# Kernel tuning notes

Measured on AMD Instinct MI355X. Metric: run time of the kernel, lower is better.

## Reference

```python
import jax, jax.numpy as jnp
import numpy as np

B, CLS, C, H, HP, WP, K = 16, 20, 512, 4, 32, 32, 9
G = H * CLS  # grapher channels = 80
EPS = 1e-5
BNS = 1.0 / np.sqrt(1.0 + EPS)  # eval-mode BN, running_mean=0, running_var=1


def _bn(x, g, b, axis):
    shape = [1] * x.ndim
    shape[axis] = -1
    return x * (g * BNS).reshape(shape) + b.reshape(shape)


def setup_inputs():
    key = jax.random.key(0)
    ks = jax.random.split(key, 16)
    def rn(k, shp, scale=0.02):
        return jax.random.normal(k, shp, dtype=jnp.float32) * scale
    return {
        "x_cls": jax.random.normal(ks[0], (B, CLS, C), jnp.float32),
        "x_patch": jax.random.normal(ks[1], (B, C, HP, WP), jnp.float32),
        "norm_x_w": jnp.ones((C, 1, 1), jnp.float32),
        "norm_x_b": jnp.zeros((C, 1, 1), jnp.float32),
        "pq_w": rn(ks[2], (C, C)), "pq_b": rn(ks[3], (C,)),
        "ncls_w": jnp.ones((C,), jnp.float32), "ncls_b": jnp.zeros((C,), jnp.float32),
        "pkv_w": rn(ks[4], (2 * C, C)), "pkv_b": rn(ks[5], (2 * C,)),
        "fc1_w": rn(ks[6], (G, G)), "fc1_b": rn(ks[7], (G,)),
        "bn1_g": jnp.ones((G,), jnp.float32), "bn1_b": jnp.zeros((G,), jnp.float32),
        "mr_w": rn(ks[8], (2 * G, 2 * G // H)), "mr_b": rn(ks[9], (2 * G,)),
        "bn2_g": jnp.ones((2 * G,), jnp.float32), "bn2_b": jnp.zeros((2 * G,), jnp.float32),
        "fc2_w": rn(ks[10], (G, 2 * G)), "fc2_b": rn(ks[11], (G,)),
        "bn3_g": jnp.ones((G,), jnp.float32), "bn3_b": jnp.zeros((G,), jnp.float32),
        "proj_w": rn(ks[12], (C, C)), "proj_b": rn(ks[13], (C,)),
    }


def _forward(x_cls, x_patch, norm_x_w, norm_x_b, pq_w, pq_b, ncls_w, ncls_b,
             pkv_w, pkv_b, fc1_w, fc1_b, bn1_g, bn1_b, mr_w, mr_b, bn2_g, bn2_b,
             fc2_w, fc2_b, bn3_g, bn3_b, proj_w, proj_b):
    hd = C // H
    N = HP * WP
    scale = hd ** -0.5
    # norm_x: LayerNormGeneral over (C,H,W)
    c0 = x_patch - x_patch.mean(axis=(1, 2, 3), keepdims=True)
    s0 = (c0 * c0).mean(axis=(1, 2, 3), keepdims=True)
    xn = c0 / jnp.sqrt(s0 + EPS) * norm_x_w + norm_x_b
    # proj_q (1x1 conv) -> multi-head query [B,H,N,hd]
    q = jnp.einsum('oc,bchw->bohw', pq_w, xn) + pq_b[None, :, None, None]
    q = q.reshape(B, H, hd, N).transpose(0, 1, 3, 2)
    # norm_cls: LayerNorm over channel dim
    m = x_cls.mean(-1, keepdims=True)
    v = ((x_cls - m) ** 2).mean(-1, keepdims=True)
    xc = (x_cls - m) / jnp.sqrt(v + EPS) * ncls_w + ncls_b
    kv = xc @ pkv_w.T + pkv_b                                  # [B,Cls,2C]
    k_, v_ = kv[..., :C], kv[..., C:]
    key_ = k_.reshape(B, CLS, H, hd).transpose(0, 2, 3, 1)     # [B,H,hd,Cls]
    val = v_.reshape(B, CLS, H, hd).transpose(0, 2, 1, 3)      # [B,H,Cls,hd]
    attn = jnp.einsum('bhnd,bhdc->bhnc', q, key_) * scale      # [B,H,N,Cls]
    amap = attn.reshape(B, H, HP, WP, CLS).transpose(0, 1, 4, 2, 3).reshape(B, G, HP, WP)
    # ---- Grapher (ViG gcn_lib): fc1 -> DyGraphConv(MRConv, KNN) -> fc2 -> residual ----
    sc = amap
    x = jnp.einsum('oc,bchw->bohw', fc1_w, amap) + fc1_b[None, :, None, None]
    x = _bn(x, bn1_g, bn1_b, 1)
    xf = x.reshape(B, G, N).transpose(0, 2, 1)                 # [B,N,G]
    # dense KNN on L2-normalized features (indices only, non-diff)
    xu = xf / jnp.maximum(jnp.linalg.norm(xf, axis=-1, keepdims=True), 1e-12)
    sq = jnp.sum(xu * xu, axis=-1)                             # [B,N]
    neg_d = 2.0 * jnp.einsum('bnc,bmc->bnm', xu, xu) - sq[:, :, None] - sq[:, None, :]
    _, nn_idx = jax.lax.top_k(neg_d, K)                        # [B,N,K]
    neigh = xf[jnp.arange(B)[:, None, None], nn_idx]           # [B,N,K,G]
    xj = jnp.max(neigh - xf[:, :, None, :], axis=2)            # [B,N,G] max-relative
    y = jnp.stack([xf, xj], axis=-1).reshape(B, N, 2 * G)      # interleave (x0,xj0,x1,...)
    # grouped 1x1 conv (groups=H), BN, GELU
    yg = y.reshape(B, N, H, 2 * G // H)
    wg = mr_w.reshape(H, 2 * G // H, 2 * G // H)
    z = jnp.einsum('bngi,goi->bngo', yg, wg).reshape(B, N, 2 * G) + mr_b
    z = _bn(z, bn2_g, bn2_b, 2)
    z = jax.nn.gelu(z, approximate=False)
    z2 = z @ fc2_w.T + fc2_b                                   # [B,N,G]
    z2 = _bn(z2, bn3_g, bn3_b, 2)
    gout = z2.transpose(0, 2, 1).reshape(B, G, HP, WP) + sc
    # ---- softmax-weighted value aggregation ----
    attn2 = gout.reshape(B, H, CLS, N).transpose(0, 1, 3, 2)   # [B,H,N,Cls]
    attn2 = jax.nn.softmax(attn2, axis=-1)
    out = jnp.einsum('bhnc,bhcd->bhnd', attn2, val)            # [B,H,N,hd]
    out = out.transpose(0, 1, 3, 2).reshape(B, C, HP, WP)
    out = jnp.einsum('oc,bchw->bohw', proj_w, out) + proj_b[None, :, None, None]
    return x_patch + out


def reference(x_cls, x_patch, norm_x_w, norm_x_b, pq_w, pq_b, ncls_w, ncls_b,
              pkv_w, pkv_b, fc1_w, fc1_b, bn1_g, bn1_b, mr_w, mr_b, bn2_g, bn2_b,
              fc2_w, fc2_b, bn3_g, bn3_b, proj_w, proj_b):
    return _forward(x_cls, x_patch, norm_x_w, norm_x_b, pq_w, pq_b, ncls_w, ncls_b,
                    pkv_w, pkv_b, fc1_w, fc1_b, bn1_g, bn1_b, mr_w, mr_b, bn2_g, bn2_b,
                    fc2_w, fc2_b, bn3_g, bn3_b, proj_w, proj_b)
```

## Files before the change

### kernel.cpp

```cpp
#include <hip/hip_runtime.h>
#include <math.h>

#define DI __device__ __forceinline__

constexpr int B_ = 16, CLS_ = 20, C_ = 512, H_ = 4, HD_ = 128, N_ = 1024, G_ = 80, G2_ = 160, K_ = 9;
constexpr float EPS_ = 1e-5f;
constexpr float BNS_ = 0.9999950000374997f;
constexpr float SCALE_ = 0.08838834764831845f;
constexpr float INVSQRT2_ = 0.7071067811865475f;

typedef __attribute__((ext_vector_type(8))) short bf16x8;
typedef __attribute__((ext_vector_type(4))) float f32x4;

constexpr long OFF_PART  = 0;
constexpr long OFF_EB    = 4096;
constexpr long OFF_EBB   = OFF_EB    + 524288;
constexpr long OFF_KV    = OFF_EBB   + 2048;
constexpr long OFF_AMAPT = OFF_KV    + 327680;
constexpr long OFF_XF    = OFF_AMAPT + 1310720;
constexpr long OFF_XUB   = OFF_XF    + 1310720;
constexpr long OFF_W1BD  = OFF_XUB   + 786432;
constexpr long OFF_FC2B  = OFF_W1BD  + 16384;
constexpr long OFF_SQ    = OFF_FC2B  + 8192;
constexpr long OFF_NEGD  = OFF_SQ    + 16384;
constexpr long OFF_GOUTT = OFF_NEGD  + 16777216 + 147456;
constexpr long OFF_WPB   = OFF_GOUTT + 1310720;
constexpr long OFF_Y     = OFF_WPB   + 131072;
constexpr long OFF_FC1B  = OFF_Y     + 1310720;
constexpr long OFF_PB    = OFF_FC1B  + 4096;

DI float wsum(float v){
#pragma unroll
  for(int d=1; d<64; d<<=1) v += __shfl_xor(v, d);
  return v;
}
DI unsigned short f2b(float f){
  unsigned u = __float_as_uint(f);
  unsigned r = (u + 0x7FFFu + ((u >> 16) & 1u)) >> 16;
  return (unsigned short)r;
}

#define GLOAD16(g, s) __builtin_amdgcn_global_load_lds((const __attribute__((address_space(1))) void*)(g), \
                        (__attribute__((address_space(3))) void*)(s), 16, 0, 0)

__global__ __launch_bounds__(256) void k_pre(const float* __restrict__ x, float* __restrict__ part,
                                             const float* __restrict__ xcls,
                                             const float* __restrict__ ncw, const float* __restrict__ ncb,
                                             const float* __restrict__ pkvw, const float* __restrict__ pkvb,
                                             float* __restrict__ kv,
                                             const float* __restrict__ projw, unsigned short* __restrict__ wpb,
                                             const float* __restrict__ mrw, const float* __restrict__ fc2w,
                                             const float* __restrict__ fc1w,
                                             unsigned short* __restrict__ w1bd, unsigned short* __restrict__ fc2b16,
                                             unsigned short* __restrict__ fc1b16){
  __shared__ float sh[CLS_*C_];
  int blk = blockIdx.x, t = threadIdx.x;
  if(blk < 1024){
    const float4* xp = (const float4*)x;
    long base4 = (long)blk * 2048;
    float s = 0.f, ss = 0.f;
#pragma unroll
    for(int j=0;j<8;++j){
      float4 v = xp[base4 + t + 256*j];
      s  += v.x + v.y + v.z + v.w;
      ss += v.x*v.x + v.y*v.y + v.z*v.z + v.w*v.w;
    }
    s = wsum(s); ss = wsum(ss);
    int wv = t >> 6;
    if((t & 63) == 0){ sh[wv] = s; sh[4+wv] = ss; }
    __syncthreads();
    if(t == 0){
      part[blk*2]   = sh[0]+sh[1]+sh[2]+sh[3];
      part[blk*2+1] = sh[4]+sh[5]+sh[6]+sh[7];
    }
    return;
  }
  if(blk < 1152){
    int idx = blk - 1024;
    int b = idx >> 3, ochunk = idx & 7;
    float (*xc)[C_] = (float(*)[C_])sh;
    int wv = t >> 6, l = t & 63;
    for(int cls = wv; cls < CLS_; cls += 4){
      const float* xr = xcls + ((long)b*CLS_ + cls) * C_;
      float vals[8];
      float s = 0.f, ss = 0.f;
#pragma unroll
      for(int j=0;j<8;++j){ float v = xr[l + 64*j]; vals[j] = v; s += v; ss += v*v; }
      s = wsum(s); ss = wsum(ss);
      float m = s / (float)C_;
      float var = ss / (float)C_ - m*m;
      float inv = 1.0f / sqrtf(var + EPS_);
#pragma unroll
      for(int j=0;j<8;++j){
        int c = l + 64*j;
        xc[cls][c] = (vals[j]-m)*inv*ncw[c] + ncb[c];
      }
    }
    __syncthreads();
    int o = ochunk*128 + (t & 127);
    int cls0 = (t >> 7) * 10;
    float acc[10] = {};
    const float* wrow = pkvw + (long)o * C_;
    for(int k4 = 0; k4 < C_; k4 += 4){
      float4 w4 = *(const float4*)&wrow[k4];
#pragma unroll
      for(int i=0;i<10;++i){
        acc[i] += w4.x*xc[cls0+i][k4] + w4.y*xc[cls0+i][k4+1] + w4.z*xc[cls0+i][k4+2] + w4.w*xc[cls0+i][k4+3];
      }
    }
    float bo = pkvb[o];
#pragma unroll
    for(int i=0;i<10;++i) kv[((long)b*CLS_ + cls0+i)*1024 + o] = acc[i] + bo;
    return;
  }
  int blk2 = blk - 1152;
  if(blk2 < 256){
    long i = (long)blk2*256 + t;
    float4 v = ((const float4*)projw)[i];
    uint2 o;
    o.x = (unsigned)f2b(v.x) | ((unsigned)f2b(v.y) << 16);
    o.y = (unsigned)f2b(v.z) | ((unsigned)f2b(v.w) << 16);
    ((uint2*)wpb)[i] = o;
    return;
  }
  int row = blk2 - 256;
  if(row < 160){
    if(t < 160){
      unsigned short v = 0;
      if(t/40 == row/40) v = f2b(mrw[row*40 + (t % 40)]);
      w1bd[row*160 + t] = v;
    }
  } else if(row < 240){
    if(t < 160) fc2b16[(row-160)*160 + t] = f2b(fc2w[(long)(row-160)*160 + t]);
  } else if(row < 320){
    int r = row - 240;
    if(t < 96) fc1b16[r*96 + t] = (t < G_) ? f2b(fc1w[(long)r*G_ + t]) : (unsigned short)0;
  }
}

__global__ __launch_bounds__(256) void k_eprep(const float* __restrict__ kv, const float* __restrict__ pqw,
                                               const float* __restrict__ pqb, const float* __restrict__ partbuf,
                                               const float* __restrict__ nw, const float* __restrict__ nbv,
                                               unsigned short* __restrict__ Eb, float* __restrict__ ebb,
                                               float* __restrict__ pb){
  int b = blockIdx.x, hh = blockIdx.y, cch = blockIdx.z, t = threadIdx.x;
  if(hh == 4){
    if(cch == 0){
      unsigned* z = (unsigned*)(Eb + ((long)b*128 + 80)*512);
      for(int i=t; i<12288; i+=256) z[i] = 0;
    }
    return;
  }
  __shared__ float sst[2];
  __shared__ float key[CLS_][HD_];
  __shared__ float part[4][CLS_][64];
  if(t < 64){
    float s  = partbuf[(b*64+t)*2];
    float ss = partbuf[(b*64+t)*2+1];
    s = wsum(s); ss = wsum(ss);
    if(t == 0){
      const float cnt = (float)(C_ * N_);
      float m = s / cnt;
      sst[0] = m;
      sst[1] = 1.0f / sqrtf(ss / cnt - m*m + EPS_);
    }
  }
  int h = hh, c0 = cch*64;
  for(int i=t; i<CLS_*HD_; i+=256){
    int cls = i >> 7, d = i & 127;
    key[cls][d] = kv[((long)b*CLS_+cls)*1024 + h*HD_ + d];
  }
  __syncthreads();
  float m = sst[0], inv = sst[1];
  int c = t & 63, ds = t >> 6;
  float acc[CLS_] = {};
  const float* wp = pqw + ((long)(h*HD_ + ds*32))*C_ + c0 + c;
#pragma unroll 8
  for(int di=0; di<32; ++di){
    float wv = wp[(long)di*C_];
#pragma unroll
    for(int cls=0; cls<CLS_; ++cls) acc[cls] += key[cls][ds*32+di]*wv;
  }
#pragma unroll
  for(int cls=0; cls<CLS_; ++cls) part[ds][cls][c] = acc[cls];
  __syncthreads();
  for(int i=t; i<CLS_*64; i+=256){
    int cls = i >> 6, cc = i & 63;
    float v = (part[0][cls][cc]+part[1][cls][cc]+part[2][cls][cc]+part[3][cls][cc]) * SCALE_;
    int cg = c0 + cc;
    float a = inv * nw[cg];
    float bbv = nbv[cg] - m*a;
    Eb[((long)b*128 + h*CLS_ + cls)*512 + cg] = f2b(v*a);
    part[0][cls][cc] = v*bbv;
  }
  __syncthreads();
  if(t < CLS_){
    float s = 0.f;
    for(int cc=0; cc<64; ++cc) s += part[0][t][cc];
    pb[((long)b*8 + cch)*G_ + t < 0 ? 0 : ((long)b*8 + cch)*G_ + h*CLS_ + t] = s;
  }
  if(cch == 0 && t >= 64 && t < 64 + CLS_){
    int tt = t - 64;
    float bacc = 0.f;
    for(int d=0; d<HD_; ++d) bacc += key[tt][d]*pqb[h*HD_+d];
    ebb[b*G_ + h*CLS_ + tt] = bacc*SCALE_;
  }
}

__global__ __launch_bounds__(256) void k_amap_fc1(const unsigned short* __restrict__ Eb,
                                                  const float* __restrict__ xp,
                                                  const float* __restrict__ ebb,
                                                  const float* __restrict__ pb,
                                                  const unsigned short* __restrict__ w1b,
                                                  const float* __restrict__ f1bias,
                                                  const float* __restrict__ g1, const float* __restrict__ b1,
                                                  float* __restrict__ amapT,
                                                  float* __restrict__ xf, unsigned short* __restrict__ xub,
                                                  float* __restrict__ sq){
  __shared__ unsigned short Xl[64*520];
  __shared__ unsigned short Bgl[4096];
  unsigned short* A1 = Xl;
  int b = blockIdx.y, n0 = blockIdx.x*64;
  int t = threadIdx.x, w = t >> 6, l = t & 63;
  int wr = w >> 1, wc = w & 1;
  {
    int nb = t & 7, cl = t >> 3;
    const float* xb = xp + (long)b*C_*N_ + n0 + nb*8;
#pragma unroll 4
    for(int pass=0; pass<16; ++pass){
      int c = pass*32 + cl;
      const float* src = xb + (long)c*N_;
      float4 v0 = *(const float4*)src;
      float4 v1 = *(const float4*)(src+4);
      int base = (nb*8)*520 + c;
      Xl[base         ] = f2b(v0.x);
      Xl[base + 520   ] = f2b(v0.y);
      Xl[base + 520*2 ] = f2b(v0.z);
      Xl[base + 520*3 ] = f2b(v0.w);
      Xl[base + 520*4 ] = f2b(v1.x);
      Xl[base + 520*5 ] = f2b(v1.y);
      Xl[base + 520*6 ] = f2b(v1.z);
      Xl[base + 520*7 ] = f2b(v1.w);
    }
  }
  __syncthreads();
  f32x4 acc[2][4] = {};
  const unsigned short* Bt = Eb + ((long)b*128 + w*16 + (l>>2))*512 + (l&3)*8;
  int ra = wr*32 + (l & 15);
  int rb = wc*64 + (l & 15);
  int kq = (l >> 4) * 8;
  for(int k0 = 0; k0 < 512; k0 += 32){
    if(k0) __syncthreads();
    GLOAD16(Bt + k0,          &Bgl[w*512]);
    GLOAD16(Bt + 64*512 + k0, &Bgl[2048 + w*512]);
    __syncthreads();
    bf16x8 af[2], bfr[4];
#pragma unroll
    for(int rt=0; rt<2; ++rt) af[rt]  = *(const bf16x8*)&Xl[(ra + rt*16)*520 + k0 + kq];
#pragma unroll
    for(int ct=0; ct<4; ++ct) bfr[ct] = *(const bf16x8*)&Bgl[(rb + ct*16)*32 + kq];
#pragma unroll
    for(int rt=0; rt<2; ++rt)
#pragma unroll
      for(int ct=0; ct<4; ++ct)
        acc[rt][ct] = __builtin_amdgcn_mfma_f32_16x16x32_bf16(af[rt], bfr[ct], acc[rt][ct], 0, 0, 0);
  }
  float bias4[4];
#pragma unroll
  for(int ct=0; ct<4; ++ct){
    int g = wc*64 + ct*16 + (l & 15);
    float bi = 0.f;
    if(g < G_){
      bi = ebb[b*G_ + g];
#pragma unroll
      for(int cc=0; cc<8; ++cc) bi += pb[((long)b*8 + cc)*G_ + g];
    }
    bias4[ct] = bi;
  }
  __syncthreads();
  int r0 = (l >> 4)*4;
#pragma unroll
  for(int rt=0; rt<2; ++rt){
#pragma unroll
    for(int r=0; r<4; ++r){
      int lrow = wr*32 + rt*16 + r0 + r;
      long rowb = ((long)b*N_ + n0 + lrow)*G_;
#pragma unroll
      for(int ct=0; ct<4; ++ct){
        int g = wc*64 + ct*16 + (l & 15);
        if(g < G_){
          float val = acc[rt][ct][r] + bias4[ct];
          amapT[rowb + g] = val;
          A1[lrow*96 + g] = f2b(val);
        } else if(g < 96){
          A1[lrow*96 + g] = 0;
        }
      }
    }
  }
  __syncthreads();
  int lr = l & 15, lk = l >> 4;
  bf16x8 ay[3];
  const unsigned short* arow = &A1[(w*16 + lr)*96 + lk*8];
#pragma unroll
  for(int ks=0; ks<3; ++ks) ay[ks] = *(const bf16x8*)&arow[ks*32];
  f32x4 acc5[5] = {};
  const unsigned short* wrow = w1b + (long)lr*96 + lk*8;
#pragma unroll
  for(int ks=0; ks<3; ++ks){
#pragma unroll
    for(int ct=0; ct<5; ++ct){
      bf16x8 bw = *(const bf16x8*)&wrow[ct*16*96 + ks*32];
      acc5[ct] = __builtin_amdgcn_mfma_f32_16x16x32_bf16(ay[ks], bw, acc5[ct], 0, 0, 0);
    }
  }
  float v[5][4];
  float ssq[4] = {0.f,0.f,0.f,0.f};
#pragma unroll
  for(int ct=0; ct<5; ++ct){
    int o = ct*16 + lr;
    float bi = f1bias[o], ga = g1[o]*BNS_, bb = b1[o];
#pragma unroll
    for(int i=0;i<4;++i){
      float vv = (acc5[ct][i] + bi)*ga + bb;
      v[ct][i] = vv;
      ssq[i] += vv*vv;
    }
  }
#pragma unroll
  for(int d=1; d<16; d<<=1){
#pragma unroll
    for(int i=0;i<4;++i) ssq[i] += __shfl_xor(ssq[i], d);
  }
  long row0g = (long)b*N_ + n0 + w*16;
#pragma unroll
  for(int i=0;i<4;++i){
    long row = row0g + lk*4 + i;
    float invn = 1.0f / fmaxf(sqrtf(ssq[i]), 1e-12f);
#pragma unroll
    for(int ct=0; ct<5; ++ct){
      int o = ct*16 + lr;
      xf[row*G_ + o] = v[ct][i];
      xub[row*96 + o] = f2b(v[ct][i]*invn);
    }
    xub[row*96 + 80 + lr] = 0;
    if(lr == 0) sq[row] = ssq[i]*invn*invn;
  }
}

template<bool RES>
__global__ __launch_bounds__(256) void k_gemm_mfma(const unsigned short* __restrict__ Wb,
                                                   const unsigned short* __restrict__ Xb,
                                                   const float* __restrict__ bias,
                                                   const float* __restrict__ Res,
                                                   float* __restrict__ Out){
  __shared__ unsigned short Al[4096];
  __shared__ unsigned short Bl[4096];
  int b = blockIdx.z;
  int o0 = blockIdx.y*128, n0 = blockIdx.x*128;
  int t = threadIdx.x, w = t >> 6, l = t & 63;
  int wr = w >> 1, wc = w & 1;
  f32x4 acc[4][4] = {};
  const unsigned short* Wt = Wb + (long)(o0 + w*16 + (l>>2))*512 + (l&3)*8;
  const unsigned short* Xt = Xb + ((long)b*N_ + n0 + w*16 + (l>>2))*512 + (l&3)*8;
  int ra = wr*64 + (l & 15);
  int rb = wc*64 + (l & 15);
  int kq = (l >> 4) * 8;
  for(int k0 = 0; k0 < 512; k0 += 32){
    if(k0) __syncthreads();
    GLOAD16(Wt + k0,            &Al[w*512]);
    GLOAD16(Wt + 64*512 + k0,   &Al[2048 + w*512]);
    GLOAD16(Xt + k0,            &Bl[w*512]);
    GLOAD16(Xt + 64*512 + k0,   &Bl[2048 + w*512]);
    __syncthreads();
    bf16x8 af[4], bfr[4];
#pragma unroll
    for(int i=0;i<4;++i){
      af[i]  = *(const bf16x8*)&Al[(ra + i*16)*32 + kq];
      bfr[i] = *(const bf16x8*)&Bl[(rb + i*16)*32 + kq];
    }
#pragma unroll
    for(int mi=0; mi<4; ++mi)
#pragma unroll
      for(int ni=0; ni<4; ++ni)
        acc[mi][ni] = __builtin_amdgcn_mfma_f32_16x16x32_bf16(af[mi], bfr[ni], acc[mi][ni], 0, 0, 0);
  }
  long obase = ((long)b*C_ + o0 + wr*64)*N_ + n0 + wc*64 + (l & 15);
  int r0 = (l >> 4) * 4;
#pragma unroll
  for(int mi=0; mi<4; ++mi){
#pragma unroll
    for(int r=0; r<4; ++r){
      int row = mi*16 + r0 + r;
      float bi = bias[o0 + wr*64 + row];
#pragma unroll
      for(int ni=0; ni<4; ++ni){
        long oi = obase + (long)row*N_ + ni*16;
        float v = acc[mi][ni][r] + bi;
        if(RES) v += Res[oi];
        Out[oi] = v;
      }
    }
  }
}

__global__ __launch_bounds__(256) void k_negd_mfma(const unsigned short* __restrict__ xub,
                                                   const float* __restrict__ sq,
                                                   float* __restrict__ negd){
  __shared__ unsigned short Al[128*96];
  __shared__ unsigned short Bl[128*96];
  int b = blockIdx.z;
  int n0 = blockIdx.y*128, m0 = blockIdx.x*128;
  int t = threadIdx.x, w = t >> 6, l = t & 63;
  int wr = w >> 1, wc = w & 1;
  const unsigned short* gA = xub + ((long)b*N_ + n0)*96;
  const unsigned short* gB = xub + ((long)b*N_ + m0)*96;
#pragma unroll
  for(int rd=0; rd<6; ++rd){
    int chunk = rd*4 + w;
    GLOAD16(gA + chunk*512 + l*8, &Al[chunk*512]);
    GLOAD16(gB + chunk*512 + l*8, &Bl[chunk*512]);
  }
  __syncthreads();
  f32x4 acc[4][4] = {};
  int ra = wr*64 + (l & 15);
  int rb = wc*64 + (l & 15);
#pragma unroll
  for(int ks=0; ks<3; ++ks){
    int kq = ks*32 + (l >> 4)*8;
    bf16x8 af[4], bfr[4];
#pragma unroll
    for(int i=0;i<4;++i){
      af[i]  = *(const bf16x8*)&Al[(ra + i*16)*96 + kq];
      bfr[i] = *(const bf16x8*)&Bl[(rb + i*16)*96 + kq];
    }
#pragma unroll
    for(int mi=0; mi<4; ++mi)
#pragma unroll
      for(int ni=0; ni<4; ++ni)
        acc[mi][ni] = __builtin_amdgcn_mfma_f32_16x16x32_bf16(af[mi], bfr[ni], acc[mi][ni], 0, 0, 0);
  }
  int r0 = (l >> 4)*4;
  const float* sqb = sq + (long)b*N_;
#pragma unroll
  for(int mi=0; mi<4; ++mi){
#pragma unroll
    for(int r=0; r<4; ++r){
      int n = n0 + wr*64 + mi*16 + r0 + r;
      float sn = sqb[n];
      long row = ((long)b*N_ + n)*N_;
#pragma unroll
      for(int ni=0; ni<4; ++ni){
        int m = m0 + wc*64 + ni*16 + (l & 15);
        negd[row + m] = 2.f*acc[mi][ni][r] - sn - sqb[m];
      }
    }
  }
}

__global__ __launch_bounds__(256) void k_topk_y(const float* __restrict__ negd, const float* __restrict__ xf,
                                                unsigned short* __restrict__ y){
  int t = threadIdx.x, wv = t >> 6, l = t & 63;
  long r = (long)blockIdx.x*4 + wv;
  long b = r >> 10;
  const float* row = negd + r*N_;
  float vals[16];
#pragma unroll
  for(int j=0;j<16;++j) vals[j] = row[l + 64*j];
  int nbs[K_];
#pragma unroll
  for(int p=0; p<K_; ++p){
    float bv = vals[0]; int bj = 0;
#pragma unroll
    for(int j=1;j<16;++j) if(vals[j] > bv){ bv = vals[j]; bj = j; }
    int bm = l + 64*bj;
#pragma unroll
    for(int d=1; d<64; d<<=1){
      float ov = __shfl_xor(bv, d);
      int   om = __shfl_xor(bm, d);
      if(ov > bv || (ov == bv && om < bm)){ bv = ov; bm = om; }
    }
    nbs[p] = bm;
#pragma unroll
    for(int j=0;j<16;++j) if(bm == l + 64*j) vals[j] = -INFINITY;
  }
  const float* frow = xf + r*G_;
  int o2s = (l < 16) ? (64 + l) : 0;
  float f0 = frow[l];
  float f1 = frow[o2s];
  float m0 = -INFINITY, m1 = -INFINITY;
#pragma unroll
  for(int k=0;k<K_;++k){
    const float* nr = xf + ((long)b*N_ + nbs[k])*G_;
    m0 = fmaxf(m0, nr[l]);
    m1 = fmaxf(m1, nr[o2s]);
  }
  unsigned short* yr = y + r*G2_;
  ushort2 u0; u0.x = f2b(f0); u0.y = f2b(m0 - f0);
  *(ushort2*)&yr[2*l] = u0;
  if(l < 16){
    ushort2 u1; u1.x = f2b(f1); u1.y = f2b(m1 - f1);
    *(ushort2*)&yr[128 + 2*l] = u1;
  }
}

__global__ __launch_bounds__(256) void k_mixer_mfma(const unsigned short* __restrict__ y,
                                                    const unsigned short* __restrict__ w1bd,
                                                    const float* __restrict__ mrb,
                                                    const float* __restrict__ g2, const float* __restrict__ b2,
                                                    const unsigned short* __restrict__ fc2b16,
                                                    const float* __restrict__ fc2bias,
                                                    const float* __restrict__ g3, const float* __restrict__ b3,
                                                    const float* __restrict__ amapT, float* __restrict__ goutT){
  __shared__ unsigned short zl[4][16][G2_];
  int t = threadIdx.x, w = t >> 6, l = t & 63;
  long row0 = ((long)blockIdx.x*4 + w)*16;
  int lr = l & 15, lk = l >> 4;
  bf16x8 ay[5];
  const unsigned short* yrow = y + (row0 + lr)*G2_ + lk*8;
#pragma unroll
  for(int ks=0; ks<5; ++ks) ay[ks] = *(const bf16x8*)&yrow[ks*32];
  f32x4 accz[10] = {};
  const unsigned short* wb = w1bd + (long)lr*G2_ + lk*8;
#pragma unroll
  for(int ks=0; ks<5; ++ks){
#pragma unroll
    for(int ct=0; ct<10; ++ct){
      bf16x8 bw = *(const bf16x8*)&wb[ct*16*G2_ + ks*32];
      accz[ct] = __builtin_amdgcn_mfma_f32_16x16x32_bf16(ay[ks], bw, accz[ct], 0, 0, 0);
    }
  }
#pragma unroll
  for(int ct=0; ct<10; ++ct){
    int o = ct*16 + lr;
    float bi = mrb[o], ga = g2[o]*BNS_, bb = b2[o];
#pragma unroll
    for(int i=0;i<4;++i){
      float v = (accz[ct][i] + bi)*ga + bb;
      float zz = v * 0.5f * (1.0f + erff(v * INVSQRT2_));
      zl[w][lk*4 + i][o] = f2b(zz);
    }
  }
  __syncthreads();
  bf16x8 az[5];
#pragma unroll
  for(int ks=0; ks<5; ++ks) az[ks] = *(const bf16x8*)&zl[w][lr][ks*32 + lk*8];
  f32x4 acc2[5] = {};
  const unsigned short* fb = fc2b16 + (long)lr*G2_ + lk*8;
#pragma unroll
  for(int ks=0; ks<5; ++ks){
#pragma unroll
    for(int ct=0; ct<5; ++ct){
      bf16x8 bw = *(const bf16x8*)&fb[ct*16*G2_ + ks*32];
      acc2[ct] = __builtin_amdgcn_mfma_f32_16x16x32_bf16(az[ks], bw, acc2[ct], 0, 0, 0);
    }
  }
#pragma unroll
  for(int ct=0; ct<5; ++ct){
    int o = ct*16 + lr;
    float bi = fc2bias[o], ga = g3[o]*BNS_, bb = b3[o];
#pragma unroll
    for(int i=0;i<4;++i){
      long row = row0 + lk*4 + i;
      float v = (acc2[ct][i] + bi)*ga + bb + amapT[row*G_ + o];
      goutT[row*G_ + o] = v;
    }
  }
}

__global__ __launch_bounds__(256) void k_softmax_pv(const float* __restrict__ goutT, const float* __restrict__ kv,
                                                    unsigned short* __restrict__ aob){
  int bh = blockIdx.x; int b = bh >> 2, h = bh & 3;
  int n0 = blockIdx.y * 64;
  __shared__ unsigned short Vt[128*32];
  __shared__ unsigned short Pl[64*40];
  __shared__ unsigned short Os[64*132];
  int t = threadIdx.x, w = t >> 6, l = t & 63;
  if(t < 128){
    int d = t;
    const float* vb = kv + ((long)b*CLS_)*1024 + C_ + h*HD_ + d;
#pragma unroll
    for(int cls=0; cls<CLS_; ++cls) Vt[d*32+cls] = f2b(vb[(long)cls*1024]);
#pragma unroll
    for(int cls=CLS_; cls<32; ++cls) Vt[d*32+cls] = 0;
  }
  if(t < 64){
    int n = n0 + t;
    const float* gr = goutT + ((long)b*N_ + n)*G_ + h*CLS_;
    float x[CLS_];
    float mx = -INFINITY;
#pragma unroll
    for(int cls=0; cls<CLS_; ++cls){ x[cls] = gr[cls]; mx = fmaxf(mx, x[cls]); }
    float s = 0.f;
#pragma unroll
    for(int cls=0; cls<CLS_; ++cls){ x[cls] = expf(x[cls]-mx); s += x[cls]; }
    float inv = 1.0f / s;
#pragma unroll
    for(int cls=0; cls<CLS_; ++cls) Pl[t*40+cls] = f2b(x[cls]*inv);
#pragma unroll
    for(int cls=CLS_; cls<32; ++cls) Pl[t*40+cls] = 0;
  }
  __syncthreads();
  int lr = l & 15, kq = (l >> 4)*8;
  f32x4 acc[4][2] = {};
  bf16x8 af[4], bf2[2];
#pragma unroll
  for(int rt=0; rt<4; ++rt) af[rt] = *(const bf16x8*)&Pl[(rt*16+lr)*40 + kq];
#pragma unroll
  for(int ci=0; ci<2; ++ci) bf2[ci] = *(const bf16x8*)&Vt[((2*w+ci)*16+lr)*32 + kq];
#pragma unroll
  for(int rt=0; rt<4; ++rt)
#pragma unroll
    for(int ci=0; ci<2; ++ci)
      acc[rt][ci] = __builtin_amdgcn_mfma_f32_16x16x32_bf16(af[rt], bf2[ci], acc[rt][ci], 0, 0, 0);
  int r0 = (l >> 4)*4;
#pragma unroll
  for(int rt=0; rt<4; ++rt)
#pragma unroll
    for(int ci=0; ci<2; ++ci)
#pragma unroll
      for(int i=0; i<4; ++i)
        Os[(rt*16 + r0 + i)*132 + (2*w+ci)*16 + lr] = f2b(acc[rt][ci][i]);
  __syncthreads();
  unsigned short* ob = aob + ((long)b*N_ + n0)*C_ + h*HD_;
#pragma unroll
  for(int j=0; j<8; ++j){
    int idx = t + 256*j;
    int row = idx >> 5, ch = idx & 31;
    *(ushort4*)&ob[(long)row*C_ + ch*4] =
        *(const ushort4*)&Os[row*132 + ch*4];
  }
}

extern "C" void kernel_launch(void* const* d_in, const int* in_sizes, int n_in,
                              void* d_out, int out_size, void* d_ws, size_t ws_size,
                              hipStream_t stream){
  const float* x_cls   = (const float*)d_in[0];
  const float* x_patch = (const float*)d_in[1];
  const float* norm_x_w = (const float*)d_in[2];
  const float* norm_x_b = (const float*)d_in[3];
  const float* pq_w  = (const float*)d_in[4];
  const float* pq_b  = (const float*)d_in[5];
  const float* ncls_w = (const float*)d_in[6];
  const float* ncls_b = (const float*)d_in[7];
  const float* pkv_w = (const float*)d_in[8];
  const float* pkv_b = (const float*)d_in[9];
  const float* fc1_w = (const float*)d_in[10];
  const float* fc1_b = (const float*)d_in[11];
  const float* bn1_g = (const float*)d_in[12];
  const float* bn1_b = (const float*)d_in[13];
  const float* mr_w  = (const float*)d_in[14];
  const float* mr_b  = (const float*)d_in[15];
  const float* bn2_g = (const float*)d_in[16];
  const float* bn2_b = (const float*)d_in[17];
  const float* fc2_w = (const float*)d_in[18];
  const float* fc2_b = (const float*)d_in[19];
  const float* bn3_g = (const float*)d_in[20];
  const float* bn3_b = (const float*)d_in[21];
  const float* proj_w = (const float*)d_in[22];
  const float* proj_b = (const float*)d_in[23];

  float* ws = (float*)d_ws;
  float* part   = ws + OFF_PART;
  float* ebb    = ws + OFF_EBB;
  float* kvbuf  = ws + OFF_KV;
  float* amapT  = ws + OFF_AMAPT;
  float* xf     = ws + OFF_XF;
  float* sqbuf  = ws + OFF_SQ;
  float* negd   = ws + OFF_NEGD;
  float* goutT  = ws + OFF_GOUTT;
  float* pbuf   = ws + OFF_PB;
  unsigned short* Eb     = (unsigned short*)(ws + OFF_EB);
  unsigned short* xub    = (unsigned short*)(ws + OFF_XUB);
  unsigned short* w1bd   = (unsigned short*)(ws + OFF_W1BD);
  unsigned short* fc2b16 = (unsigned short*)(ws + OFF_FC2B);
  unsigned short* ybuf   = (unsigned short*)(ws + OFF_Y);
  unsigned short* fc1b16 = (unsigned short*)(ws + OFF_FC1B);
  unsigned short* aob = (unsigned short*)(ws + OFF_NEGD);
  unsigned short* wpb = (unsigned short*)(ws + OFF_WPB);
  float* out = (float*)d_out;

  k_pre<<<1728, 256, 0, stream>>>(x_patch, part, x_cls, ncls_w, ncls_b, pkv_w, pkv_b, kvbuf,
                                  proj_w, wpb, mr_w, fc2_w, fc1_w, w1bd, fc2b16, fc1b16);
  k_eprep<<<dim3(16,5,8), 256, 0, stream>>>(kvbuf, pq_w, pq_b, part, norm_x_w, norm_x_b, Eb, ebb, pbuf);
  k_amap_fc1<<<dim3(16,16), 256, 0, stream>>>(Eb, x_patch, ebb, pbuf, fc1b16, fc1_b, bn1_g, bn1_b,
                                              amapT, xf, xub, sqbuf);
  k_negd_mfma<<<dim3(8,8,16), 256, 0, stream>>>(xub, sqbuf, negd);
  k_topk_y<<<4096, 256, 0, stream>>>(negd, xf, ybuf);
  k_mixer_mfma<<<256, 256, 0, stream>>>(ybuf, w1bd, mr_b, bn2_g, bn2_b,
                                        fc2b16, fc2_b, bn3_g, bn3_b, amapT, goutT);
  k_softmax_pv<<<dim3(64,16), 256, 0, stream>>>(goutT, kvbuf, aob);
  k_gemm_mfma<true><<<dim3(8,4,16), 256, 0, stream>>>(wpb, aob, proj_b, x_patch, out);
}
```

Before: 174.3 us.

## Move class-token KV projection to a separate bf16 MFMA kernel

```diff
diff --git a/kernel.cpp b/kernel.cpp
--- a/kernel.cpp
+++ b/kernel.cpp
@@ -28,6 +28,8 @@
 constexpr long OFF_Y     = OFF_WPB   + 131072;
 constexpr long OFF_FC1B  = OFF_Y     + 1310720;
 constexpr long OFF_PB    = OFF_FC1B  + 4096;
+constexpr long OFF_XCB   = OFF_PB    + 10240;
+constexpr long OFF_PKVB  = OFF_XCB   + 131072;
 
 DI float wsum(float v){
 #pragma unroll
@@ -46,14 +48,14 @@
 __global__ __launch_bounds__(256) void k_pre(const float* __restrict__ x, float* __restrict__ part,
                                              const float* __restrict__ xcls,
                                              const float* __restrict__ ncw, const float* __restrict__ ncb,
-                                             const float* __restrict__ pkvw, const float* __restrict__ pkvb,
-                                             float* __restrict__ kv,
+                                             unsigned short* __restrict__ xcb,
+                                             const float* __restrict__ pkvw, unsigned short* __restrict__ pkvb16,
                                              const float* __restrict__ projw, unsigned short* __restrict__ wpb,
                                              const float* __restrict__ mrw, const float* __restrict__ fc2w,
                                              const float* __restrict__ fc1w,
                                              unsigned short* __restrict__ w1bd, unsigned short* __restrict__ fc2b16,
                                              unsigned short* __restrict__ fc1b16){
-  __shared__ float sh[CLS_*C_];
+  __shared__ float rs[4], rss[4];
   int blk = blockIdx.x, t = threadIdx.x;
   if(blk < 1024){
     const float4* xp = (const float4*)x;
@@ -67,55 +69,43 @@
     }
     s = wsum(s); ss = wsum(ss);
     int wv = t >> 6;
-    if((t & 63) == 0){ sh[wv] = s; sh[4+wv] = ss; }
+    if((t & 63) == 0){ rs[wv] = s; rss[wv] = ss; }
     __syncthreads();
     if(t == 0){
-      part[blk*2]   = sh[0]+sh[1]+sh[2]+sh[3];
-      part[blk*2+1] = sh[4]+sh[5]+sh[6]+sh[7];
+      part[blk*2]   = rs[0]+rs[1]+rs[2]+rs[3];
+      part[blk*2+1] = rss[0]+rss[1]+rss[2]+rss[3];
     }
     return;
   }
-  if(blk < 1152){
-    int idx = blk - 1024;
-    int b = idx >> 3, ochunk = idx & 7;
-    float (*xc)[C_] = (float(*)[C_])sh;
+  if(blk < 1040){
+    int b = blk - 1024;
     int wv = t >> 6, l = t & 63;
-    for(int cls = wv; cls < CLS_; cls += 4){
-      const float* xr = xcls + ((long)b*CLS_ + cls) * C_;
-      float vals[8];
-      float s = 0.f, ss = 0.f;
-#pragma unroll
-      for(int j=0;j<8;++j){ float v = xr[l + 64*j]; vals[j] = v; s += v; ss += v*v; }
-      s = wsum(s); ss = wsum(ss);
-      float m = s / (float)C_;
-      float var = ss / (float)C_ - m*m;
-      float inv = 1.0f / sqrtf(var + EPS_);
-#pragma unroll
-      for(int j=0;j<8;++j){
-        int c = l + 64*j;
-        xc[cls][c] = (vals[j]-m)*inv*ncw[c] + ncb[c];
+    for(int cls = wv; cls < 32; cls += 4){
+      unsigned short* orow = xcb + ((long)b*32 + cls)*512;
+      if(cls < CLS_){
+        const float* xr = xcls + ((long)b*CLS_ + cls) * C_;
+        float vals[8];
+        float s = 0.f, ss = 0.f;
+#pragma unroll
+        for(int j=0;j<8;++j){ float v = xr[l + 64*j]; vals[j] = v; s += v; ss += v*v; }
+        s = wsum(s); ss = wsum(ss);
+        float m = s / (float)C_;
+        float var = ss / (float)C_ - m*m;
+        float inv = 1.0f / sqrtf(var + EPS_);
+#pragma unroll
+        for(int j=0;j<8;++j){
+          int c = l + 64*j;
+          orow[c] = f2b((vals[j]-m)*inv*ncw[c] + ncb[c]);
+        }
+      } else {
+#pragma unroll
+        for(int j=0;j<8;++j) orow[l + 64*j] = 0;
       }
     }
-    __syncthreads();
-    int o = ochunk*128 + (t & 127);
-    int cls0 = (t >> 7) * 10;
-    float acc[10] = {};
-    const float* wrow = pkvw + (long)o * C_;
-    for(int k4 = 0; k4 < C_; k4 += 4){
-      float4 w4 = *(const float4*)&wrow[k4];
-#pragma unroll
-      for(int i=0;i<10;++i){
-        acc[i] += w4.x*xc[cls0+i][k4] + w4.y*xc[cls0+i][k4+1] + w4.z*xc[cls0+i][k4+2] + w4.w*xc[cls0+i][k4+3];
-      }
-    }
-    float bo = pkvb[o];
-#pragma unroll
-    for(int i=0;i<10;++i) kv[((long)b*CLS_ + cls0+i)*1024 + o] = acc[i] + bo;
     return;
   }
-  int blk2 = blk - 1152;
-  if(blk2 < 256){
-    long i = (long)blk2*256 + t;
+  if(blk < 1296){
+    long i = (long)(blk - 1040)*256 + t;
     float4 v = ((const float4*)projw)[i];
     uint2 o;
     o.x = (unsigned)f2b(v.x) | ((unsigned)f2b(v.y) << 16);
@@ -123,7 +113,16 @@
     ((uint2*)wpb)[i] = o;
     return;
   }
-  int row = blk2 - 256;
+  if(blk < 1808){
+    long i = (long)(blk - 1296)*256 + t;
+    float4 v = ((const float4*)pkvw)[i];
+    uint2 o;
+    o.x = (unsigned)f2b(v.x) | ((unsigned)f2b(v.y) << 16);
+    o.y = (unsigned)f2b(v.z) | ((unsigned)f2b(v.w) << 16);
+    ((uint2*)pkvb16)[i] = o;
+    return;
+  }
+  int row = blk - 1808;
   if(row < 160){
     if(t < 160){
       unsigned short v = 0;
@@ -135,6 +134,51 @@
   } else if(row < 320){
     int r = row - 240;
     if(t < 96) fc1b16[r*96 + t] = (t < G_) ? f2b(fc1w[(long)r*G_ + t]) : (unsigned short)0;
+  }
+}
+
+__global__ __launch_bounds__(256) void k_kv_mfma(const unsigned short* __restrict__ xcb,
+                                                 const unsigned short* __restrict__ pkvb16,
+                                                 const float* __restrict__ pkvb,
+                                                 float* __restrict__ kv){
+  __shared__ unsigned short Al[4096];
+  __shared__ unsigned short Bl[1024];
+  int b = blockIdx.x >> 3, o0 = (blockIdx.x & 7)*128;
+  int t = threadIdx.x, w = t >> 6, l = t & 63;
+  f32x4 acc[2][2] = {};
+  const unsigned short* At = pkvb16 + (long)(o0 + w*16 + (l>>2))*512 + (l&3)*8;
+  const unsigned short* Bt = xcb + ((long)b*32 + w*16 + (l>>2))*512 + (l&3)*8;
+  int kq = (l >> 4)*8;
+  for(int k0 = 0; k0 < 512; k0 += 32){
+    if(k0) __syncthreads();
+    GLOAD16(At + k0,          &Al[w*512]);
+    GLOAD16(At + 64*512 + k0, &Al[2048 + w*512]);
+    if(w < 2) GLOAD16(Bt + k0, &Bl[w*512]);
+    __syncthreads();
+    bf16x8 af[2], bfr[2];
+#pragma unroll
+    for(int mi=0; mi<2; ++mi) af[mi]  = *(const bf16x8*)&Al[(w*32 + mi*16 + (l & 15))*32 + kq];
+#pragma unroll
+    for(int ni=0; ni<2; ++ni) bfr[ni] = *(const bf16x8*)&Bl[(ni*16 + (l & 15))*32 + kq];
+#pragma unroll
+    for(int mi=0; mi<2; ++mi)
+#pragma unroll
+      for(int ni=0; ni<2; ++ni)
+        acc[mi][ni] = __builtin_amdgcn_mfma_f32_16x16x32_bf16(af[mi], bfr[ni], acc[mi][ni], 0, 0, 0);
+  }
+  int r0 = (l >> 4)*4;
+#pragma unroll
+  for(int mi=0; mi<2; ++mi){
+#pragma unroll
+    for(int r=0; r<4; ++r){
+      int o = o0 + w*32 + mi*16 + r0 + r;
+      float bi = pkvb[o];
+#pragma unroll
+      for(int ni=0; ni<2; ++ni){
+        int cls = ni*16 + (l & 15);
+        if(cls < CLS_) kv[((long)b*CLS_ + cls)*1024 + o] = acc[mi][ni][r] + bi;
+      }
+    }
   }
 }
 
@@ -197,7 +241,7 @@
   if(t < CLS_){
     float s = 0.f;
     for(int cc=0; cc<64; ++cc) s += part[0][t][cc];
-    pb[((long)b*8 + cch)*G_ + t < 0 ? 0 : ((long)b*8 + cch)*G_ + h*CLS_ + t] = s;
+    pb[((long)b*8 + cch)*G_ + h*CLS_ + t] = s;
   }
   if(cch == 0 && t >= 64 && t < 64 + CLS_){
     int tt = t - 64;
@@ -676,12 +720,16 @@
   unsigned short* fc2b16 = (unsigned short*)(ws + OFF_FC2B);
   unsigned short* ybuf   = (unsigned short*)(ws + OFF_Y);
   unsigned short* fc1b16 = (unsigned short*)(ws + OFF_FC1B);
+  unsigned short* xcb    = (unsigned short*)(ws + OFF_XCB);
+  unsigned short* pkvb16 = (unsigned short*)(ws + OFF_PKVB);
   unsigned short* aob = (unsigned short*)(ws + OFF_NEGD);
   unsigned short* wpb = (unsigned short*)(ws + OFF_WPB);
   float* out = (float*)d_out;
 
-  k_pre<<<1728, 256, 0, stream>>>(x_patch, part, x_cls, ncls_w, ncls_b, pkv_w, pkv_b, kvbuf,
-                                  proj_w, wpb, mr_w, fc2_w, fc1_w, w1bd, fc2b16, fc1b16);
+  k_pre<<<2128, 256, 0, stream>>>(x_patch, part, x_cls, ncls_w, ncls_b, xcb,
+                                  pkv_w, pkvb16, proj_w, wpb,
+                                  mr_w, fc2_w, fc1_w, w1bd, fc2b16, fc1b16);
+  k_kv_mfma<<<128, 256, 0, stream>>>(xcb, pkvb16, pkv_b, kvbuf);
   k_eprep<<<dim3(16,5,8), 256, 0, stream>>>(kvbuf, pq_w, pq_b, part, norm_x_w, norm_x_b, Eb, ebb, pbuf);
   k_amap_fc1<<<dim3(16,16), 256, 0, stream>>>(Eb, x_patch, ebb, pbuf, fc1b16, fc1_b, bn1_g, bn1_b,
                                               amapT, xf, xub, sqbuf);
```

Result: faster. 162.3 us (-6.9%).
